# Optimization experiments

Hardware: AMD Instinct MI355X
Metric: run time of the kernel (lower is better)

## Reference

```python
import jax, jax.numpy as jnp
import numpy as np

B, L, P, T, D, H = 16, 50, 49, 20, 512, 8
DH = D // H
DFF = 4 * D
EPS = 1e-6
NEG = -1000000000.0


def gelu_tanh(x):
    return 0.5 * x * (1.0 + jnp.tanh(jnp.sqrt(2.0 / jnp.pi) * (x + 0.044715 * x ** 3)))


def layernorm(x, a, b):
    # torch LayerNorm (custom): unbiased std, divide by (std + eps)
    mean = jnp.mean(x, axis=-1, keepdims=True)
    std = jnp.sqrt(jnp.var(x, axis=-1, keepdims=True, ddof=1))
    return a * (x - mean) / (std + EPS) + b


def setup_inputs() -> dict:
    key = jax.random.key(0)
    ks = jax.random.split(key, 20)
    s = 0.02
    return {
        "img": jax.random.normal(ks[0], (B, L, P, D), jnp.float32),
        "title": jax.random.normal(ks[1], (B, L, T, D), jnp.float32),
        "mask": jax.random.randint(ks[2], (B, L, T), 0, 2, jnp.int32),
        "scale_img": jax.random.normal(ks[3], (H, P), jnp.float32) * 0.1,
        "scale_title": jax.random.normal(ks[4], (H, T), jnp.float32) * 0.1,
        "w_proj": jax.random.normal(ks[5], (D, D), jnp.float32) * s,
        "b_proj": jnp.zeros((D,), jnp.float32),
        "w1_img": jax.random.normal(ks[6], (DFF, D), jnp.float32) * s,
        "b1_img": jnp.zeros((DFF,), jnp.float32),
        "w2_img": jax.random.normal(ks[7], (D, DFF), jnp.float32) * s,
        "b2_img": jnp.zeros((D,), jnp.float32),
        "w1_tit": jax.random.normal(ks[8], (DFF, D), jnp.float32) * s,
        "b1_tit": jnp.zeros((DFF,), jnp.float32),
        "w2_tit": jax.random.normal(ks[9], (D, DFF), jnp.float32) * s,
        "b2_tit": jnp.zeros((D,), jnp.float32),
        "ln_a_img": jnp.ones((D,), jnp.float32),
        "ln_b_img": jnp.zeros((D,), jnp.float32),
        "ln_a_tit": jnp.ones((D,), jnp.float32),
        "ln_b_tit": jnp.zeros((D,), jnp.float32),
    }


def _forward(img, title, mask, scale_img, scale_title, w_proj, b_proj,
             w1_img, b1_img, w2_img, b2_img, w1_tit, b1_tit, w2_tit, b2_tit,
             ln_a_img, ln_b_img, ln_a_tit, ln_b_tit):
    imgh = img.reshape(B, L, P, H, DH)      # [B,L,P,H,dh]
    tith = title.reshape(B, L, T, H, DH)    # [B,L,T,H,dh]

    raw = jnp.einsum('blphd,blthd->blhpt', imgh, tith) / jnp.sqrt(jnp.float32(DH))
    # corr_title is the transpose of the UNSCALED corr_img
    corr_img = raw * scale_img[None, None, :, :, None]                     # [B,L,H,P,T]
    corr_tit = jnp.swapaxes(raw, -1, -2) * scale_title[None, None, :, :, None]  # [B,L,H,T,P]

    m_img = mask[:, :, None, None, :]  # [B,L,1,1,T] -> broadcast over H,P
    m_tit = mask[:, :, None, :, None]  # [B,L,1,T,1]
    corr_img = jnp.where(m_img == 0, NEG, corr_img)
    corr_tit = jnp.where(m_tit == 0, NEG, corr_tit)

    p_img = jax.nn.softmax(corr_img, axis=-1)  # [B,L,H,P,T]
    p_tit = jax.nn.softmax(corr_tit, axis=-1)  # [B,L,H,T,P]

    # T != P, so the torch code takes the else branch (swapped outputs)
    hid_img = jnp.einsum('blhtp,blphd->blthd', p_tit, imgh).reshape(B, L, T, D)
    hid_tit = jnp.einsum('blhpt,blthd->blphd', p_img, tith).reshape(B, L, P, D)

    # both projected with img_layer (faithful to source)
    hid_img = hid_img @ w_proj.T + b_proj
    hid_tit = hid_tit @ w_proj.T + b_proj

    ffn_img = gelu_tanh(hid_img @ w1_img.T + b1_img) @ w2_img.T + b2_img
    ffn_tit = gelu_tanh(hid_tit @ w1_tit.T + b1_tit) @ w2_tit.T + b2_tit

    out_img = hid_img + layernorm(ffn_img, ln_a_img, ln_b_img)
    out_tit = hid_tit + layernorm(ffn_tit, ln_a_tit, ln_b_tit)
    return out_img, out_tit


def reference(img, title, mask, scale_img, scale_title, w_proj, b_proj,
              w1_img, b1_img, w2_img, b2_img, w1_tit, b1_tit, w2_tit, b2_tit,
              ln_a_img, ln_b_img, ln_a_tit, ln_b_tit):
    return _forward(img, title, mask, scale_img, scale_title, w_proj, b_proj,
                    w1_img, b1_img, w2_img, b2_img, w1_tit, b1_tit, w2_tit, b2_tit,
                    ln_a_img, ln_b_img, ln_a_tit, ln_b_tit)
```

## Files before the change

kernel.cpp:

```cpp
#include <hip/hip_runtime.h>
#include <hip/hip_bf16.h>

#define BB   16
#define LL   50
#define PP   49
#define TT   20
#define DD   512
#define HH   8
#define DHH  64
#define DFF  2048

#define BL     (BB*LL)
#define ROWS_I (BL*TT)
#define ROWS_T (BL*PP)
#define ROWS_A (ROWS_I+ROWS_T)
#define OUT_I_ELEMS ((size_t)ROWS_I*DD)
#define CHUNK 19600

#define R1_OFF 80281600ull
#define R2_OFF 136806400ull
#define R3_OFF 176947200ull

typedef __attribute__((ext_vector_type(8))) short bf16x8;
typedef __attribute__((ext_vector_type(4))) float f32x4;

__device__ __forceinline__ unsigned short f2bf(float f) {
    union { float f; unsigned int i; } w; w.f = f;
    unsigned int x = w.i;
    unsigned int r = (x + 0x7fffu + ((x >> 16) & 1u)) >> 16;
    return (unsigned short)r;
}
__device__ __forceinline__ float gelu_tanh_f(float x) {
    float c = 0.7978845608028654f * (x + 0.044715f * x * x * x);
    return 0.5f * x * (1.0f + tanhf(c));
}

__global__ __launch_bounds__(256) void cvt_kernel(
    const float* __restrict__ s, unsigned short* __restrict__ d, int n4)
{
    int i = blockIdx.x * 256 + threadIdx.x;
    if (i < n4) {
        float4 v = ((const float4*)s)[i];
        ushort4 u;
        u.x = f2bf(v.x); u.y = f2bf(v.y); u.z = f2bf(v.z); u.w = f2bf(v.w);
        ((ushort4*)d)[i] = u;
    }
}

__global__ __launch_bounds__(256) void attn_kernel(
    const float* __restrict__ img, const float* __restrict__ title,
    const int* __restrict__ mask, const float* __restrict__ scale_img,
    const float* __restrict__ scale_tit, unsigned short* __restrict__ hid)
{
    const int blh = blockIdx.x;
    const int h  = blh & 7;
    const int bl = blh >> 3;
    const int tid = threadIdx.x;
    const int wave = tid >> 6;
    const int lane = tid & 63;

    __shared__ __align__(16) float simg[PP][68];
    __shared__ __align__(16) float stit[TT][68];
    __shared__ __align__(16) float S [PP][TT];
    __shared__ __align__(16) float pI[PP][TT];
    __shared__ __align__(16) float pT[TT][52];
    __shared__ int   msk[TT];

    const float* imgbase = img   + (size_t)bl * PP * DD + h * DHH;
    const float* titbase = title + (size_t)bl * TT * DD + h * DHH;

    for (int i = tid; i < PP * 16; i += 256) {
        int p = i >> 4, d4 = i & 15;
        *(float4*)&simg[p][d4 * 4] = *(const float4*)(imgbase + (size_t)p * DD + d4 * 4);
    }
    for (int i = tid; i < TT * 16; i += 256) {
        int t = i >> 4, d4 = i & 15;
        *(float4*)&stit[t][d4 * 4] = *(const float4*)(titbase + (size_t)t * DD + d4 * 4);
    }
    if (tid < TT) msk[tid] = mask[bl * TT + tid];
    __syncthreads();

    if (tid < PP * 5) {
        const int p  = tid / 5;
        const int tg = tid - p * 5;
        float a0 = 0.f, a1 = 0.f, a2 = 0.f, a3 = 0.f;
        #pragma unroll 4
        for (int d = 0; d < DHH; d += 4) {
            float4 a  = *(const float4*)&simg[p][d];
            float4 b0 = *(const float4*)&stit[tg     ][d];
            float4 b1 = *(const float4*)&stit[tg +  5][d];
            float4 b2 = *(const float4*)&stit[tg + 10][d];
            float4 b3 = *(const float4*)&stit[tg + 15][d];
            a0 += a.x*b0.x + a.y*b0.y + a.z*b0.z + a.w*b0.w;
            a1 += a.x*b1.x + a.y*b1.y + a.z*b1.z + a.w*b1.w;
            a2 += a.x*b2.x + a.y*b2.y + a.z*b2.z + a.w*b2.w;
            a3 += a.x*b3.x + a.y*b3.y + a.z*b3.z + a.w*b3.w;
        }
        S[p][tg     ] = a0 * 0.125f;
        S[p][tg +  5] = a1 * 0.125f;
        S[p][tg + 10] = a2 * 0.125f;
        S[p][tg + 15] = a3 * 0.125f;
    }
    __syncthreads();

    if (tid < PP) {
        const int p = tid;
        const float sc = scale_img[h * PP + p];
        float m = -1e30f;
        #pragma unroll
        for (int t = 0; t < TT; ++t) {
            float x = (msk[t] == 0) ? -1e9f : S[p][t] * sc;
            m = fmaxf(m, x);
        }
        float sum = 0.f;
        #pragma unroll
        for (int t = 0; t < TT; ++t) {
            float x = (msk[t] == 0) ? -1e9f : S[p][t] * sc;
            float e = __expf(x - m);
            pI[p][t] = e; sum += e;
        }
        float inv = 1.f / sum;
        #pragma unroll
        for (int t = 0; t < TT; ++t) pI[p][t] *= inv;
    }
    if (tid >= 64 && tid < 64 + TT) {
        const int t = tid - 64;
        const float sc = scale_tit[h * TT + t];
        const bool dead = (msk[t] == 0);
        float m = -1e30f;
        #pragma unroll
        for (int p = 0; p < PP; ++p) {
            float x = dead ? -1e9f : S[p][t] * sc;
            m = fmaxf(m, x);
        }
        float sum = 0.f;
        #pragma unroll
        for (int p = 0; p < PP; ++p) {
            float x = dead ? -1e9f : S[p][t] * sc;
            float e = __expf(x - m);
            pT[t][p] = e; sum += e;
        }
        float inv = 1.f / sum;
        #pragma unroll
        for (int p = 0; p < PP; ++p) pT[t][p] *= inv;
    }
    __syncthreads();

    {
        float accA[5] = {0.f, 0.f, 0.f, 0.f, 0.f};
        #pragma unroll
        for (int p = 0; p < 48; p += 4) {
            float v0 = simg[p + 0][lane];
            float v1 = simg[p + 1][lane];
            float v2 = simg[p + 2][lane];
            float v3 = simg[p + 3][lane];
            #pragma unroll
            for (int j = 0; j < 5; ++j) {
                const int t = wave + j * 4;
                float4 w4 = *(const float4*)&pT[t][p];
                accA[j] += v0 * w4.x + v1 * w4.y + v2 * w4.z + v3 * w4.w;
            }
        }
        {
            float v0 = simg[48][lane];
            #pragma unroll
            for (int j = 0; j < 5; ++j)
                accA[j] += v0 * pT[wave + j * 4][48];
        }
        #pragma unroll
        for (int j = 0; j < 5; ++j) {
            const int t = wave + j * 4;
            hid[(size_t)(bl * TT + t) * DD + h * DHH + lane] = f2bf(accA[j]);
        }
    }

    {
        float accB[13] = {0.f,0.f,0.f,0.f,0.f,0.f,0.f,0.f,0.f,0.f,0.f,0.f,0.f};
        #pragma unroll
        for (int t = 0; t < TT; t += 4) {
            float v0 = stit[t + 0][lane];
            float v1 = stit[t + 1][lane];
            float v2 = stit[t + 2][lane];
            float v3 = stit[t + 3][lane];
            #pragma unroll
            for (int j = 0; j < 13; ++j) {
                const int p = wave + j * 4;
                if (p < PP) {
                    float4 w4 = *(const float4*)&pI[p][t];
                    accB[j] += v0 * w4.x + v1 * w4.y + v2 * w4.z + v3 * w4.w;
                }
            }
        }
        #pragma unroll
        for (int j = 0; j < 13; ++j) {
            const int p = wave + j * 4;
            if (p < PP)
                hid[OUT_I_ELEMS + (size_t)(bl * PP + p) * DD + h * DHH + lane] = f2bf(accB[j]);
        }
    }
}

template<bool GELU, bool F32OUT, bool BF16OUT>
__global__ __launch_bounds__(256) void gemm_mfma(
    const unsigned short* __restrict__ A, const unsigned short* __restrict__ Bw,
    const float* __restrict__ bias,
    float* __restrict__ Cf, unsigned short* __restrict__ Cb,
    int M, int N, int K)
{
    __shared__ unsigned short As[128 * 32];
    __shared__ unsigned short Bs[128 * 32];
    const int tid  = threadIdx.x;
    const int wave = tid >> 6;
    const int lane = tid & 63;
    const int row0 = blockIdx.y * 128;
    const int col0 = blockIdx.x * 128;
    const int m_off = (wave >> 1) * 64;
    const int n_off = (wave & 1) * 64;
    const int lane_m = lane & 15;
    const int lane_k = (lane >> 4) * 8;

    f32x4 acc[4][4] = {};

    for (int k0 = 0; k0 < K; k0 += 32) {
        #pragma unroll
        for (int q = 0; q < 2; ++q) {
            const int li = q * 256 + tid;
            int gr = row0 + (li >> 2);
            if (gr >= M) gr = M - 1;
            const unsigned short* gp = A + (size_t)gr * K + k0 + (li & 3) * 8;
            __builtin_amdgcn_global_load_lds(
                (const __attribute__((address_space(1))) unsigned int*)gp,
                (__attribute__((address_space(3))) unsigned int*)&As[li * 8], 16, 0, 0);
        }
        #pragma unroll
        for (int q = 0; q < 2; ++q) {
            const int li = q * 256 + tid;
            const unsigned short* gp = Bw + (size_t)(col0 + (li >> 2)) * K + k0 + (li & 3) * 8;
            __builtin_amdgcn_global_load_lds(
                (const __attribute__((address_space(1))) unsigned int*)gp,
                (__attribute__((address_space(3))) unsigned int*)&Bs[li * 8], 16, 0, 0);
        }
        __syncthreads();

        bf16x8 af[4], bf[4];
        #pragma unroll
        for (int i = 0; i < 4; ++i) {
            af[i] = *(const bf16x8*)&As[(m_off + i * 16 + lane_m) * 32 + lane_k];
            bf[i] = *(const bf16x8*)&Bs[(n_off + i * 16 + lane_m) * 32 + lane_k];
        }
        #pragma unroll
        for (int i = 0; i < 4; ++i)
            #pragma unroll
            for (int j = 0; j < 4; ++j)
                acc[i][j] = __builtin_amdgcn_mfma_f32_16x16x32_bf16(af[i], bf[j], acc[i][j], 0, 0, 0);
        __syncthreads();
    }

    #pragma unroll
    for (int i = 0; i < 4; ++i) {
        #pragma unroll
        for (int r = 0; r < 4; ++r) {
            const int row = row0 + m_off + i * 16 + (lane >> 4) * 4 + r;
            if (row < M) {
                #pragma unroll
                for (int j = 0; j < 4; ++j) {
                    const int col = col0 + n_off + j * 16 + lane_m;
                    float v = acc[i][j][r] + bias[col];
                    if (GELU) v = gelu_tanh_f(v);
                    if (F32OUT)  Cf[(size_t)row * N + col] = v;
                    if (BF16OUT) Cb[(size_t)row * N + col] = f2bf(v);
                }
            }
        }
    }
}

__global__ __launch_bounds__(256) void ln_res_kernel(
    const float* __restrict__ f2, float* __restrict__ out,
    const float* __restrict__ a, const float* __restrict__ b, int M)
{
    const int wave = threadIdx.x >> 6;
    const int lane = threadIdx.x & 63;
    const int row = blockIdx.x * 4 + wave;
    if (row >= M) return;
    const float* x = f2 + (size_t)row * DD;
    float* o = out + (size_t)row * DD;

    float xs[8];
    float s1 = 0.f, s2 = 0.f;
    #pragma unroll
    for (int i = 0; i < 8; ++i) {
        float v = x[lane + i * 64];
        xs[i] = v; s1 += v; s2 += v * v;
    }
    #pragma unroll
    for (int off = 32; off > 0; off >>= 1) {
        s1 += __shfl_xor(s1, off, 64);
        s2 += __shfl_xor(s2, off, 64);
    }
    const float mean = s1 * (1.f / 512.f);
    float var = (s2 - 512.f * mean * mean) * (1.f / 511.f);
    var = fmaxf(var, 0.f);
    const float rinv = 1.f / (sqrtf(var) + 1e-6f);
    #pragma unroll
    for (int i = 0; i < 8; ++i) {
        const int d = lane + i * 64;
        o[d] = o[d] + a[d] * (xs[i] - mean) * rinv + b[d];
    }
}

extern "C" void kernel_launch(void* const* d_in, const int* in_sizes, int n_in,
                              void* d_out, int out_size, void* d_ws, size_t ws_size,
                              hipStream_t stream) {
    const float* img       = (const float*)d_in[0];
    const float* title     = (const float*)d_in[1];
    const int*   mask      = (const int*)  d_in[2];
    const float* scale_img = (const float*)d_in[3];
    const float* scale_tit = (const float*)d_in[4];
    const float* w_proj    = (const float*)d_in[5];
    const float* b_proj    = (const float*)d_in[6];
    const float* w1_img    = (const float*)d_in[7];
    const float* b1_img    = (const float*)d_in[8];
    const float* w2_img    = (const float*)d_in[9];
    const float* b2_img    = (const float*)d_in[10];
    const float* w1_tit    = (const float*)d_in[11];
    const float* b1_tit    = (const float*)d_in[12];
    const float* w2_tit    = (const float*)d_in[13];
    const float* b2_tit    = (const float*)d_in[14];
    const float* ln_a_img  = (const float*)d_in[15];
    const float* ln_b_img  = (const float*)d_in[16];
    const float* ln_a_tit  = (const float*)d_in[17];
    const float* ln_b_tit  = (const float*)d_in[18];

    float* out = (float*)d_out;
    unsigned short* hid_bf = (unsigned short*)d_ws;
    unsigned short* act    = (unsigned short*)d_ws;
    unsigned short* out_bf = (unsigned short*)((char*)d_ws + R1_OFF);
    float*          f2     = (float*)((char*)d_ws + R2_OFF);
    unsigned short* wp_bf  = (unsigned short*)((char*)d_ws + R3_OFF);
    unsigned short* w1i_bf = wp_bf  + 262144;
    unsigned short* w2i_bf = w1i_bf + 1048576;
    unsigned short* w1t_bf = w2i_bf + 1048576;
    unsigned short* w2t_bf = w1t_bf + 1048576;

    cvt_kernel<<<(262144/4 + 255)/256, 256, 0, stream>>>(w_proj, wp_bf, 262144/4);
    cvt_kernel<<<(1048576/4 + 255)/256, 256, 0, stream>>>(w1_img, w1i_bf, 1048576/4);
    cvt_kernel<<<(1048576/4 + 255)/256, 256, 0, stream>>>(w2_img, w2i_bf, 1048576/4);
    cvt_kernel<<<(1048576/4 + 255)/256, 256, 0, stream>>>(w1_tit, w1t_bf, 1048576/4);
    cvt_kernel<<<(1048576/4 + 255)/256, 256, 0, stream>>>(w2_tit, w2t_bf, 1048576/4);

    attn_kernel<<<BL * HH, 256, 0, stream>>>(img, title, mask, scale_img, scale_tit, hid_bf);

    gemm_mfma<false, true, true><<<dim3(DD/128, (ROWS_A + 127)/128), 256, 0, stream>>>(
        hid_bf, wp_bf, b_proj, out, out_bf, ROWS_A, DD, DD);

    gemm_mfma<true, false, true><<<dim3(DFF/128, (ROWS_I + 127)/128), 256, 0, stream>>>(
        out_bf, w1i_bf, b1_img, nullptr, act, ROWS_I, DFF, DD);
    gemm_mfma<false, true, false><<<dim3(DD/128, (ROWS_I + 127)/128), 256, 0, stream>>>(
        act, w2i_bf, b2_img, f2, nullptr, ROWS_I, DD, DFF);
    ln_res_kernel<<<(ROWS_I + 3)/4, 256, 0, stream>>>(f2, out, ln_a_img, ln_b_img, ROWS_I);

    for (int c = 0; c < 2; ++c) {
        const unsigned short* a1 = out_bf + (size_t)(ROWS_I + c * CHUNK) * DD;
        float* o1 = out + OUT_I_ELEMS + (size_t)c * CHUNK * DD;
        gemm_mfma<true, false, true><<<dim3(DFF/128, (CHUNK + 127)/128), 256, 0, stream>>>(
            a1, w1t_bf, b1_tit, nullptr, act, CHUNK, DFF, DD);
        gemm_mfma<false, true, false><<<dim3(DD/128, (CHUNK + 127)/128), 256, 0, stream>>>(
            act, w2t_bf, b2_tit, f2, nullptr, CHUNK, DD, DFF);
        ln_res_kernel<<<(CHUNK + 3)/4, 256, 0, stream>>>(f2, o1, ln_a_tit, ln_b_tit, CHUNK);
    }
}
```

Before: 906.1 us.

## Double-buffer GEMM LDS tiles with XOR swizzle and use exp-based GELU

Rewrites the MFMA GEMM main loop to double-buffer the A/B LDS tiles, so the next k-slice's global-to-LDS loads are issued before computing on the current one, and it keeps a single barrier per iteration. It also XOR-swizzles the 16-byte chunk placement in LDS to reduce bank conflicts on fragment reads, and hoists address arithmetic out of the loop. GELU tanh is rewritten as x*sigmoid(2c) using __expf, which is mathematically equivalent but cheaper. LDS usage doubles, which may reduce occupancy, and the fast exp slightly changes numerics.

Result: faster. 828.7 us (-8.5%).

```diff
diff --git a/kernel.cpp b/kernel.cpp
--- a/kernel.cpp
+++ b/kernel.cpp
@@ -30,9 +30,9 @@
     unsigned int r = (x + 0x7fffu + ((x >> 16) & 1u)) >> 16;
     return (unsigned short)r;
 }
-__device__ __forceinline__ float gelu_tanh_f(float x) {
-    float c = 0.7978845608028654f * (x + 0.044715f * x * x * x);
-    return 0.5f * x * (1.0f + tanhf(c));
+__device__ __forceinline__ float gelu_fast(float x) {
+    float c2 = 1.5957691216057308f * (x + 0.044715f * x * x * x);
+    return x / (1.0f + __expf(-c2));
 }
 
 __global__ __launch_bounds__(256) void cvt_kernel(
@@ -207,8 +207,8 @@
     float* __restrict__ Cf, unsigned short* __restrict__ Cb,
     int M, int N, int K)
 {
-    __shared__ unsigned short As[128 * 32];
-    __shared__ unsigned short Bs[128 * 32];
+    __shared__ unsigned short As[2][128 * 32];
+    __shared__ unsigned short Bs[2][128 * 32];
     const int tid  = threadIdx.x;
     const int wave = tid >> 6;
     const int lane = tid & 63;
@@ -217,44 +217,65 @@
     const int m_off = (wave >> 1) * 64;
     const int n_off = (wave & 1) * 64;
     const int lane_m = lane & 15;
-    const int lane_k = (lane >> 4) * 8;
+
+    const int slot8 = (((lane >> 4) ^ ((lane_m >> 1) & 3)) * 8);
+
+    const int li0 = tid, li1 = 256 + tid;
+    const int r0 = li0 >> 2, r1 = li1 >> 2;
+    const int c80 = (li0 & 3) ^ ((r0 >> 1) & 3);
+    const int c81 = (li1 & 3) ^ ((r1 >> 1) & 3);
+    int grA0 = row0 + r0; if (grA0 >= M) grA0 = M - 1;
+    int grA1 = row0 + r1; if (grA1 >= M) grA1 = M - 1;
+    const unsigned short* aP0 = A  + (size_t)grA0 * K + c80 * 8;
+    const unsigned short* aP1 = A  + (size_t)grA1 * K + c81 * 8;
+    const unsigned short* bP0 = Bw + (size_t)(col0 + r0) * K + c80 * 8;
+    const unsigned short* bP1 = Bw + (size_t)(col0 + r1) * K + c81 * 8;
 
     f32x4 acc[4][4] = {};
 
-    for (int k0 = 0; k0 < K; k0 += 32) {
-        #pragma unroll
-        for (int q = 0; q < 2; ++q) {
-            const int li = q * 256 + tid;
-            int gr = row0 + (li >> 2);
-            if (gr >= M) gr = M - 1;
-            const unsigned short* gp = A + (size_t)gr * K + k0 + (li & 3) * 8;
-            __builtin_amdgcn_global_load_lds(
-                (const __attribute__((address_space(1))) unsigned int*)gp,
-                (__attribute__((address_space(3))) unsigned int*)&As[li * 8], 16, 0, 0);
-        }
-        #pragma unroll
-        for (int q = 0; q < 2; ++q) {
-            const int li = q * 256 + tid;
-            const unsigned short* gp = Bw + (size_t)(col0 + (li >> 2)) * K + k0 + (li & 3) * 8;
-            __builtin_amdgcn_global_load_lds(
-                (const __attribute__((address_space(1))) unsigned int*)gp,
-                (__attribute__((address_space(3))) unsigned int*)&Bs[li * 8], 16, 0, 0);
-        }
-        __syncthreads();
-
-        bf16x8 af[4], bf[4];
+    #define STAGE(buf, k0)                                                          \
+        do {                                                                        \
+            __builtin_amdgcn_global_load_lds(                                       \
+                (const __attribute__((address_space(1))) unsigned int*)(aP0 + (k0)),\
+                (__attribute__((address_space(3))) unsigned int*)&As[buf][li0 * 8], \
+                16, 0, 0);                                                          \
+            __builtin_amdgcn_global_load_lds(                                       \
+                (const __attribute__((address_space(1))) unsigned int*)(aP1 + (k0)),\
+                (__attribute__((address_space(3))) unsigned int*)&As[buf][li1 * 8], \
+                16, 0, 0);                                                          \
+            __builtin_amdgcn_global_load_lds(                                       \
+                (const __attribute__((address_space(1))) unsigned int*)(bP0 + (k0)),\
+                (__attribute__((address_space(3))) unsigned int*)&Bs[buf][li0 * 8], \
+                16, 0, 0);                                                          \
+            __builtin_amdgcn_global_load_lds(                                       \
+                (const __attribute__((address_space(1))) unsigned int*)(bP1 + (k0)),\
+                (__attribute__((address_space(3))) unsigned int*)&Bs[buf][li1 * 8], \
+                16, 0, 0);                                                          \
+        } while (0)
+
+    STAGE(0, 0);
+    __syncthreads();
+
+    const int nk = K >> 5;
+    for (int t = 0; t < nk; ++t) {
+        const int cur = t & 1;
+        if (t + 1 < nk) STAGE(cur ^ 1, (t + 1) * 32);
+
+        bf16x8 af[4], bfr[4];
         #pragma unroll
         for (int i = 0; i < 4; ++i) {
-            af[i] = *(const bf16x8*)&As[(m_off + i * 16 + lane_m) * 32 + lane_k];
-            bf[i] = *(const bf16x8*)&Bs[(n_off + i * 16 + lane_m) * 32 + lane_k];
+            af[i]  = *(const bf16x8*)&As[cur][(m_off + i * 16 + lane_m) * 32 + slot8];
+            bfr[i] = *(const bf16x8*)&Bs[cur][(n_off + i * 16 + lane_m) * 32 + slot8];
         }
         #pragma unroll
         for (int i = 0; i < 4; ++i)
             #pragma unroll
             for (int j = 0; j < 4; ++j)
-                acc[i][j] = __builtin_amdgcn_mfma_f32_16x16x32_bf16(af[i], bf[j], acc[i][j], 0, 0, 0);
+                acc[i][j] = __builtin_amdgcn_mfma_f32_16x16x32_bf16(af[i], bfr[j], acc[i][j], 0, 0, 0);
+
         __syncthreads();
     }
+    #undef STAGE
 
     #pragma unroll
     for (int i = 0; i < 4; ++i) {
@@ -266,7 +287,7 @@
                 for (int j = 0; j < 4; ++j) {
                     const int col = col0 + n_off + j * 16 + lane_m;
                     float v = acc[i][j][r] + bias[col];
-                    if (GELU) v = gelu_tanh_f(v);
+                    if (GELU) v = gelu_fast(v);
                     if (F32OUT)  Cf[(size_t)row * N + col] = v;
                     if (BF16OUT) Cb[(size_t)row * N + col] = f2bf(v);
                 }
```

## Rewrite MFMA GEMM with 256x256 tiles, double-buffered LDS and swizzle

Applied to the files above, without the earlier changes.

Replaces the 128x128, single-buffered GEMM with a 512-thread kernel that uses 256x256 output tiles and K=64 steps. The next tile is prefetched into a second LDS buffer using explicit vmcnt waits, and LDS columns are XOR-swizzled to avoid bank conflicts. The MFMA sections also raise wave priority, and GELU is rewritten as x*sigmoid(2c) with a fast exp. The aim is more data reuse per load and hiding global-load latency behind compute. In exchange, LDS grows to 128KB per block and each wave holds 128 accumulator registers, which caps occupancy at about one block per CU. The larger tiles also waste more work on the padded last row-tile.

Result: no change. 914.1 us (+0.9%).

```diff
diff --git a/kernel.cpp b/kernel.cpp
--- a/kernel.cpp
+++ b/kernel.cpp
@@ -30,9 +30,9 @@
     unsigned int r = (x + 0x7fffu + ((x >> 16) & 1u)) >> 16;
     return (unsigned short)r;
 }
-__device__ __forceinline__ float gelu_tanh_f(float x) {
-    float c = 0.7978845608028654f * (x + 0.044715f * x * x * x);
-    return 0.5f * x * (1.0f + tanhf(c));
+__device__ __forceinline__ float gelu_fast(float x) {
+    float c2 = 1.5957691216057308f * (x + 0.044715f * x * x * x);
+    return x / (1.0f + __expf(-c2));
 }
 
 __global__ __launch_bounds__(256) void cvt_kernel(
@@ -201,72 +201,126 @@
 }
 
 template<bool GELU, bool F32OUT, bool BF16OUT>
-__global__ __launch_bounds__(256) void gemm_mfma(
+__global__ __launch_bounds__(512) void gemm_mfma(
     const unsigned short* __restrict__ A, const unsigned short* __restrict__ Bw,
     const float* __restrict__ bias,
     float* __restrict__ Cf, unsigned short* __restrict__ Cb,
     int M, int N, int K)
 {
-    __shared__ unsigned short As[128 * 32];
-    __shared__ unsigned short Bs[128 * 32];
+    __shared__ unsigned short As[2][256 * 64];
+    __shared__ unsigned short Bs[2][256 * 64];
+
     const int tid  = threadIdx.x;
-    const int wave = tid >> 6;
+    const int wid  = tid >> 6;
     const int lane = tid & 63;
-    const int row0 = blockIdx.y * 128;
-    const int col0 = blockIdx.x * 128;
-    const int m_off = (wave >> 1) * 64;
-    const int n_off = (wave & 1) * 64;
-    const int lane_m = lane & 15;
-    const int lane_k = (lane >> 4) * 8;
-
-    f32x4 acc[4][4] = {};
-
-    for (int k0 = 0; k0 < K; k0 += 32) {
-        #pragma unroll
-        for (int q = 0; q < 2; ++q) {
-            const int li = q * 256 + tid;
-            int gr = row0 + (li >> 2);
-            if (gr >= M) gr = M - 1;
-            const unsigned short* gp = A + (size_t)gr * K + k0 + (li & 3) * 8;
-            __builtin_amdgcn_global_load_lds(
-                (const __attribute__((address_space(1))) unsigned int*)gp,
-                (__attribute__((address_space(3))) unsigned int*)&As[li * 8], 16, 0, 0);
-        }
-        #pragma unroll
-        for (int q = 0; q < 2; ++q) {
-            const int li = q * 256 + tid;
-            const unsigned short* gp = Bw + (size_t)(col0 + (li >> 2)) * K + k0 + (li & 3) * 8;
-            __builtin_amdgcn_global_load_lds(
-                (const __attribute__((address_space(1))) unsigned int*)gp,
-                (__attribute__((address_space(3))) unsigned int*)&Bs[li * 8], 16, 0, 0);
-        }
-        __syncthreads();
-
-        bf16x8 af[4], bf[4];
-        #pragma unroll
-        for (int i = 0; i < 4; ++i) {
-            af[i] = *(const bf16x8*)&As[(m_off + i * 16 + lane_m) * 32 + lane_k];
-            bf[i] = *(const bf16x8*)&Bs[(n_off + i * 16 + lane_m) * 32 + lane_k];
-        }
-        #pragma unroll
-        for (int i = 0; i < 4; ++i)
+    const int wm   = wid >> 2;
+    const int wn   = wid & 3;
+    const int row0 = blockIdx.y * 256;
+    const int col0 = blockIdx.x * 256;
+    const int lm   = lane & 15;
+    const int kg   = lane >> 4;
+    const int s0   = kg ^ (lm & 7);
+
+    const int srow  = tid >> 3;
+    const int scol8 = (tid & 7) ^ (srow & 7);
+    const unsigned short* aP[4];
+    const unsigned short* bP[4];
+    #pragma unroll
+    for (int q = 0; q < 4; ++q) {
+        int ar = row0 + q * 64 + srow; if (ar >= M) ar = M - 1;
+        aP[q] = A  + (size_t)ar * K + scol8 * 8;
+        bP[q] = Bw + (size_t)(col0 + q * 64 + srow) * K + scol8 * 8;
+    }
+
+    #define STAGE(buf, kt)                                                           \
+        do {                                                                         \
+            const int koff_ = (kt) * 64;                                             \
+            _Pragma("unroll")                                                        \
+            for (int q_ = 0; q_ < 4; ++q_) {                                         \
+                __builtin_amdgcn_global_load_lds(                                    \
+                    (const __attribute__((address_space(1))) unsigned int*)(aP[q_] + koff_), \
+                    (__attribute__((address_space(3))) unsigned int*)&As[buf][(q_ * 512 + tid) * 8], \
+                    16, 0, 0);                                                       \
+                __builtin_amdgcn_global_load_lds(                                    \
+                    (const __attribute__((address_space(1))) unsigned int*)(bP[q_] + koff_), \
+                    (__attribute__((address_space(3))) unsigned int*)&Bs[buf][(q_ * 512 + tid) * 8], \
+                    16, 0, 0);                                                       \
+            }                                                                        \
+        } while (0)
+
+    f32x4 acc[8][4] = {};
+
+    const int nt = K >> 6;
+    STAGE(0, 0);
+    STAGE(1, 1);
+
+    for (int kt = 0; kt < nt; ++kt) {
+        const int cur = kt & 1;
+        if (kt + 1 < nt) asm volatile("s_waitcnt vmcnt(8)" ::: "memory");
+        else             asm volatile("s_waitcnt vmcnt(0)" ::: "memory");
+        __builtin_amdgcn_s_barrier();
+        asm volatile("" ::: "memory");
+
+        const unsigned short* Ab = &As[cur][0];
+        const unsigned short* Bb = &Bs[cur][0];
+
+        #pragma unroll
+        for (int mh = 0; mh < 2; ++mh) {
             #pragma unroll
-            for (int j = 0; j < 4; ++j)
-                acc[i][j] = __builtin_amdgcn_mfma_f32_16x16x32_bf16(af[i], bf[j], acc[i][j], 0, 0, 0);
-        __syncthreads();
-    }
-
-    #pragma unroll
-    for (int i = 0; i < 4; ++i) {
+            for (int nh = 0; nh < 2; ++nh) {
+                bf16x8 a0[4], a1[4], b0[2], b1[2];
+                #pragma unroll
+                for (int i = 0; i < 4; ++i) {
+                    const int row = wm * 128 + (mh * 4 + i) * 16 + lm;
+                    a0[i] = *(const bf16x8*)&Ab[row * 64 + s0 * 8];
+                    a1[i] = *(const bf16x8*)&Ab[row * 64 + (s0 ^ 4) * 8];
+                }
+                #pragma unroll
+                for (int j = 0; j < 2; ++j) {
+                    const int row = wn * 64 + (nh * 2 + j) * 16 + lm;
+                    b0[j] = *(const bf16x8*)&Bb[row * 64 + s0 * 8];
+                    b1[j] = *(const bf16x8*)&Bb[row * 64 + (s0 ^ 4) * 8];
+                }
+                __builtin_amdgcn_s_setprio(1);
+                #pragma unroll
+                for (int i = 0; i < 4; ++i)
+                    #pragma unroll
+                    for (int j = 0; j < 2; ++j)
+                        acc[mh*4+i][nh*2+j] = __builtin_amdgcn_mfma_f32_16x16x32_bf16(
+                            a0[i], b0[j], acc[mh*4+i][nh*2+j], 0, 0, 0);
+                #pragma unroll
+                for (int i = 0; i < 4; ++i)
+                    #pragma unroll
+                    for (int j = 0; j < 2; ++j)
+                        acc[mh*4+i][nh*2+j] = __builtin_amdgcn_mfma_f32_16x16x32_bf16(
+                            a1[i], b1[j], acc[mh*4+i][nh*2+j], 0, 0, 0);
+                __builtin_amdgcn_s_setprio(0);
+            }
+        }
+
+        asm volatile("" ::: "memory");
+        __builtin_amdgcn_s_barrier();
+        asm volatile("" ::: "memory");
+        if (kt + 2 < nt) STAGE(cur, kt + 2);
+    }
+    #undef STAGE
+
+    float bv[4];
+    #pragma unroll
+    for (int n = 0; n < 4; ++n) bv[n] = bias[col0 + wn * 64 + n * 16 + lm];
+
+    const int orow0 = row0 + wm * 128 + (lane >> 4) * 4;
+    #pragma unroll
+    for (int m = 0; m < 8; ++m) {
         #pragma unroll
         for (int r = 0; r < 4; ++r) {
-            const int row = row0 + m_off + i * 16 + (lane >> 4) * 4 + r;
+            const int row = orow0 + m * 16 + r;
             if (row < M) {
                 #pragma unroll
-                for (int j = 0; j < 4; ++j) {
-                    const int col = col0 + n_off + j * 16 + lane_m;
-                    float v = acc[i][j][r] + bias[col];
-                    if (GELU) v = gelu_tanh_f(v);
+                for (int n = 0; n < 4; ++n) {
+                    const int col = col0 + wn * 64 + n * 16 + lm;
+                    float v = acc[m][n][r] + bv[n];
+                    if (GELU) v = gelu_fast(v);
                     if (F32OUT)  Cf[(size_t)row * N + col] = v;
                     if (BF16OUT) Cb[(size_t)row * N + col] = f2bf(v);
                 }
@@ -351,21 +405,21 @@
 
     attn_kernel<<<BL * HH, 256, 0, stream>>>(img, title, mask, scale_img, scale_tit, hid_bf);
 
-    gemm_mfma<false, true, true><<<dim3(DD/128, (ROWS_A + 127)/128), 256, 0, stream>>>(
+    gemm_mfma<false, true, true><<<dim3(DD/256, (ROWS_A + 255)/256), 512, 0, stream>>>(
         hid_bf, wp_bf, b_proj, out, out_bf, ROWS_A, DD, DD);
 
-    gemm_mfma<true, false, true><<<dim3(DFF/128, (ROWS_I + 127)/128), 256, 0, stream>>>(
+    gemm_mfma<true, false, true><<<dim3(DFF/256, (ROWS_I + 255)/256), 512, 0, stream>>>(
         out_bf, w1i_bf, b1_img, nullptr, act, ROWS_I, DFF, DD);
-    gemm_mfma<false, true, false><<<dim3(DD/128, (ROWS_I + 127)/128), 256, 0, stream>>>(
+    gemm_mfma<false, true, false><<<dim3(DD/256, (ROWS_I + 255)/256), 512, 0, stream>>>(
         act, w2i_bf, b2_img, f2, nullptr, ROWS_I, DD, DFF);
     ln_res_kernel<<<(ROWS_I + 3)/4, 256, 0, stream>>>(f2, out, ln_a_img, ln_b_img, ROWS_I);
 
     for (int c = 0; c < 2; ++c) {
         const unsigned short* a1 = out_bf + (size_t)(ROWS_I + c * CHUNK) * DD;
         float* o1 = out + OUT_I_ELEMS + (size_t)c * CHUNK * DD;
-        gemm_mfma<true, false, true><<<dim3(DFF/128, (CHUNK + 127)/128), 256, 0, stream>>>(
+        gemm_mfma<true, false, true><<<dim3(DFF/256, (CHUNK + 255)/256), 512, 0, stream>>>(
             a1, w1t_bf, b1_tit, nullptr, act, CHUNK, DFF, DD);
-        gemm_mfma<false, true, false><<<dim3(DD/128, (CHUNK + 127)/128), 256, 0, stream>>>(
+        gemm_mfma<false, true, false><<<dim3(DD/256, (CHUNK + 255)/256), 512, 0, stream>>>(
             act, w2t_bf, b2_tit, f2, nullptr, CHUNK, DD, DFF);
         ln_res_kernel<<<(CHUNK + 3)/4, 256, 0, stream>>>(f2, o1, ln_a_tit, ln_b_tit, CHUNK);
     }
```
